# Performance work log

Hardware: AMD Instinct MI355X
Metric: run time of the kernel (lower is better)

Reference implementation:

```python
import jax, jax.numpy as jnp
import numpy as np

B, SQ, SKV, D = 4, 4096, 4096, 64

def setup_inputs() -> dict:
    key = jax.random.key(0)
    kq, kv = jax.random.split(key)
    query = jax.random.normal(kq, (B, SQ, D), dtype=jnp.float32)
    value = jax.random.normal(kv, (B, SKV, D), dtype=jnp.float32)
    return {"query": query, "value": value}

def reference(query, value):
    # scores = Q @ V^T  (value acts as both keys and values; no 1/sqrt(d) scaling)
    scores = jnp.einsum('bqd,bkd->bqk', query, value)  # [B, SQ, SKV]
    dist = jax.nn.softmax(scores, axis=-1)
    context = jnp.einsum('bqk,bkd->bqd', dist, value)  # [B, SQ, D]
    return context
```

## Files before the change

kernel.cpp:

```cpp
#include <hip/hip_runtime.h>
#include <type_traits>


#define NB   4
#define SQ   4096
#define SKV  4096
#define DH   64
#define L2E  1.44269504088896340736f

typedef _Float16 half8 __attribute__((ext_vector_type(8)));
typedef _Float16 half4 __attribute__((ext_vector_type(4)));
typedef _Float16 half2v __attribute__((ext_vector_type(2)));
typedef float f32x4 __attribute__((ext_vector_type(4)));
typedef unsigned short u16;

#define MFMA16(a, b, c) __builtin_amdgcn_mfma_f32_16x16x16f16((a), (b), (c), 0, 0, 0)
#define MFMA32(a, b, c) __builtin_amdgcn_mfma_f32_16x16x32_f16((a), (b), (c), 0, 0, 0)

__device__ __forceinline__ u16 f2h(float f) {
  _Float16 h = (_Float16)f;
  return __builtin_bit_cast(u16, h);
}
__device__ __forceinline__ half2v pkrtz(float a, float b) {
  return __builtin_bit_cast(half2v, __builtin_amdgcn_cvt_pkrtz(a, b));
}
__device__ __forceinline__ float fmax3(float a, float b, float c) {
  return fmaxf(fmaxf(a, b), c);
}

typedef __attribute__((address_space(1))) void gvoid;
typedef __attribute__((address_space(3))) void lvoid;
__device__ __forceinline__ void dma16(const u16* g, u16* l) {
  __builtin_amdgcn_global_load_lds((gvoid*)g, (lvoid*)l, 16, 0, 0);
}

__global__ __launch_bounds__(256) void prep_kernel(
    const float* __restrict__ V, u16* __restrict__ vh, u16* __restrict__ vt) {
  __shared__ u16 ldsT[16 * 72];
  int blk = blockIdx.x;
  int x   = blk & 7;
  int b   = x >> 1;
  int rem = ((x & 1) << 7) + (blk >> 3);
  int j0  = (rem >> 2) << 6;
  int d0  = (rem & 3) << 4;
  int t   = threadIdx.x;
  int j   = t >> 2;
  int dc  = (t & 3) << 2;

  const float* src = V + ((size_t)(b * SKV) + j0 + j) * DH + d0 + dc;
  float4 v4 = *(const float4*)src;
  u16 h[4] = {f2h(v4.x), f2h(v4.y), f2h(v4.z), f2h(v4.w)};
  unsigned p0 = (unsigned)h[0] | ((unsigned)h[1] << 16);
  unsigned p1 = (unsigned)h[2] | ((unsigned)h[3] << 16);
  int dfull = d0 + dc;
  int physd = ((((dfull >> 3) ^ (j & 7)) << 3)) + (dfull & 7);
  *(uint2*)(vh + ((size_t)(b * SKV) + j0 + j) * DH + physd) = make_uint2(p0, p1);

#pragma unroll
  for (int k = 0; k < 4; ++k) ldsT[(dc + k) * 72 + j] = h[k];
  __syncthreads();

  int dl = t >> 4;
  int jc = (t & 15) << 2;
  u16 tr[4];
#pragma unroll
  for (int k = 0; k < 4; ++k) tr[k] = ldsT[dl * 72 + jc + k];
  unsigned q0 = (unsigned)tr[0] | ((unsigned)tr[1] << 16);
  unsigned q1 = (unsigned)tr[2] | ((unsigned)tr[3] << 16);
  int d   = d0 + dl;
  int kc2 = jc >> 5;
  int g   = (jc >> 4) & 1;
  int qd  = (jc >> 2) & 3;
  int hp  = ((kc2 << 2) | qd) ^ (d & 7);
  *(uint2*)(vt + ((size_t)(b * DH) + d) * SKV + j0 + (hp << 3) + (g << 2)) =
      make_uint2(q0, q1);
}

__global__ __launch_bounds__(256, 4) void attn_kernel(
    const float* __restrict__ Q,
    const u16* __restrict__ vh,
    const u16* __restrict__ vt,
    u16* __restrict__ po,
    float* __restrict__ pm,
    float* __restrict__ pl,
    int S, int kvLen) {
  __shared__ __align__(16) u16 lds[2][2][4096];

  int blk  = blockIdx.x;
  int tile, s;
  if (S == 4) {
    int x  = blk & 7;
    int jj = ((x & 1) << 7) + (blk >> 3);
    tile   = ((x >> 1) << 6) + (jj >> 2);
    s      = jj & 3;
  } else {
    tile = blk / S;
    s    = blk - tile * S;
  }
  int b    = tile >> 6;
  int q0   = (tile & 63) << 6;
  int kv0  = s * kvLen;
  int t    = threadIdx.x;
  int wave = t >> 6;
  int lane = t & 63;
  int col  = lane & 15;
  int quad = lane >> 4;
  int qw   = q0 + (wave << 4);
  int c7   = col & 7;

  const u16* gv  = vh + (size_t)(b * SKV) * DH;
  const u16* gvt = vt + (size_t)(b * DH) * SKV;

  int r0 = t >> 3;
  int c0 = (t & 7) << 3;
  int wb = wave << 9;

  half8 qf[2];
#pragma unroll
  for (int kc = 0; kc < 2; ++kc) {
    const float* qp = Q + ((size_t)(b * SQ) + qw + col) * DH + kc * 32 + (quad << 3);
    float4 a0 = *(const float4*)qp;
    float4 a1 = *(const float4*)(qp + 4);
    half8 hq;
    hq[0] = (_Float16)(a0.x * L2E); hq[1] = (_Float16)(a0.y * L2E);
    hq[2] = (_Float16)(a0.z * L2E); hq[3] = (_Float16)(a0.w * L2E);
    hq[4] = (_Float16)(a1.x * L2E); hq[5] = (_Float16)(a1.y * L2E);
    hq[6] = (_Float16)(a1.z * L2E); hq[7] = (_Float16)(a1.w * L2E);
    qf[kc] = hq;
  }

  f32x4 o[4];
#pragma unroll
  for (int nf = 0; nf < 4; ++nf) o[nf] = (f32x4){0.f, 0.f, 0.f, 0.f};
  float m_r = -1e30f, l_r = 0.f;

  half4 pf[4];
  half8 vr[8];

  int ch0 = quad ^ c7;
  int ch1 = ch0 ^ 4;
  const char* Lb = (const char*)&lds[0][0][0];
  const char* a0p = Lb + (col << 7) + (ch0 << 4);
  const char* a1p = Lb + (col << 7) + (ch1 << 4);

  const u16* pvh  = gv + ((size_t)(kv0 + r0) << 6) + c0;
  const u16* pvh2 = pvh + 2048;
  const u16* pvt  = gvt + (size_t)r0 * SKV + kv0 + c0;
  const u16* pvt2 = pvt + (size_t)32 * SKV;

  dma16(pvh,  &lds[0][0][0] + wb);
  dma16(pvh2, &lds[0][0][0] + 2048 + wb);
  dma16(pvt,  &lds[0][1][0] + wb);
  dma16(pvt2, &lds[0][1][0] + 2048 + wb);
  pvh += 4096; pvh2 += 4096; pvt += 64; pvt2 += 64;

  int nIter = kvLen >> 6;

  auto body = [&](auto BUFC, int it_) {
    constexpr int BUF = decltype(BUFC)::value;
    constexpr int BO  = BUF * 16384;
    __syncthreads();

    if (it_ + 1 < nIter) {
      dma16(pvh,  &lds[BUF ^ 1][0][0] + wb);
      dma16(pvh2, &lds[BUF ^ 1][0][0] + 2048 + wb);
      dma16(pvt,  &lds[BUF ^ 1][1][0] + wb);
      dma16(pvt2, &lds[BUF ^ 1][1][0] + 2048 + wb);
    }
    pvh += 4096; pvh2 += 4096; pvt += 64; pvt2 += 64;

    f32x4 sf[4];
#pragma unroll
    for (int nf = 0; nf < 4; ++nf) sf[nf] = (f32x4){0.f, 0.f, 0.f, 0.f};
    __builtin_amdgcn_s_setprio(1);
#pragma unroll
    for (int nf = 0; nf < 4; ++nf) {
      half8 av0 = *(const half8*)(a0p + BO + nf * 2048);
      sf[nf] = MFMA32(av0, qf[0], sf[nf]);
      half8 av1 = *(const half8*)(a1p + BO + nf * 2048);
      sf[nf] = MFMA32(av1, qf[1], sf[nf]);
    }
    __builtin_amdgcn_s_setprio(0);

    float t0 = fmax3(sf[0][0], sf[0][1], sf[0][2]);
    float t1 = fmax3(sf[0][3], sf[1][0], sf[1][1]);
    float t2 = fmax3(sf[1][2], sf[1][3], sf[2][0]);
    float t3 = fmax3(sf[2][1], sf[2][2], sf[2][3]);
    float t4 = fmax3(sf[3][0], sf[3][1], sf[3][2]);
    float t5 = fmax3(t0, t1, sf[3][3]);
    float tmw = fmax3(t2, t3, t4);
    tmw = fmaxf(tmw, t5);
    float tx = __shfl_xor(tmw, 16, 64);

    if (it_ > 0) {
      __builtin_amdgcn_s_setprio(1);
#pragma unroll
      for (int nf2 = 0; nf2 < 4; ++nf2) {
        half8 w8 = vr[nf2];
        half4 wlo = __builtin_shufflevector(w8, w8, 0, 1, 2, 3);
        half4 whi = __builtin_shufflevector(w8, w8, 4, 5, 6, 7);
        o[nf2] = MFMA16(wlo, pf[0], o[nf2]);
        o[nf2] = MFMA16(whi, pf[1], o[nf2]);
      }
      __builtin_amdgcn_s_setprio(0);
    }

    float tm2 = fmaxf(tmw, tx);
    float ty = __shfl_xor(tm2, 32, 64);

    if (it_ > 0) {
      __builtin_amdgcn_s_setprio(1);
#pragma unroll
      for (int nf2 = 0; nf2 < 4; ++nf2) {
        half8 w8 = vr[4 + nf2];
        half4 wlo = __builtin_shufflevector(w8, w8, 0, 1, 2, 3);
        half4 whi = __builtin_shufflevector(w8, w8, 4, 5, 6, 7);
        o[nf2] = MFMA16(wlo, pf[2], o[nf2]);
        o[nf2] = MFMA16(whi, pf[3], o[nf2]);
      }
      __builtin_amdgcn_s_setprio(0);
    }

    {
      float tm = fmaxf(tm2, ty);
      float mn = fmaxf(m_r, tm);
      float al = 1.0f;
      bool need = !__all(mn == m_r);
      if (need) {
        al = exp2f(m_r - mn);
        m_r = mn;
      }
      float rs = 0.f;
#pragma unroll
      for (int nf = 0; nf < 4; ++nf) {
        float p0 = exp2f(sf[nf][0] - mn);
        float p1 = exp2f(sf[nf][1] - mn);
        float p2 = exp2f(sf[nf][2] - mn);
        float p3 = exp2f(sf[nf][3] - mn);
        rs += (p0 + p1) + (p2 + p3);
        half2v lo = pkrtz(p0, p1);
        half2v hi = pkrtz(p2, p3);
        pf[nf] = __builtin_shufflevector(lo, hi, 0, 1, 2, 3);
      }
      if (need) {
#pragma unroll
        for (int nf = 0; nf < 4; ++nf)
#pragma unroll
          for (int r = 0; r < 4; ++r) o[nf][r] *= al;
      }
      l_r = l_r * al + rs;
    }

#pragma unroll
    for (int nf2 = 0; nf2 < 4; ++nf2) {
      vr[nf2]     = *(const half8*)(a0p + BO + 8192 + nf2 * 2048);
      vr[4 + nf2] = *(const half8*)(a1p + BO + 8192 + nf2 * 2048);
    }
  };

  for (int it = 0; it < nIter; it += 2) {
    body(std::integral_constant<int, 0>{}, it);
    body(std::integral_constant<int, 1>{}, it + 1);
  }

  __builtin_amdgcn_s_setprio(1);
#pragma unroll
  for (int kc2 = 0; kc2 < 2; ++kc2) {
#pragma unroll
    for (int nf2 = 0; nf2 < 4; ++nf2) {
      half8 w8 = vr[kc2 * 4 + nf2];
      half4 wlo = __builtin_shufflevector(w8, w8, 0, 1, 2, 3);
      half4 whi = __builtin_shufflevector(w8, w8, 4, 5, 6, 7);
      o[nf2] = MFMA16(wlo, pf[kc2 * 2], o[nf2]);
      o[nf2] = MFMA16(whi, pf[kc2 * 2 + 1], o[nf2]);
    }
  }
  __builtin_amdgcn_s_setprio(0);

  l_r += __shfl_xor(l_r, 16, 64);
  l_r += __shfl_xor(l_r, 32, 64);
  int pidx = tile * S + s;
  if (quad == 0) {
    pm[(size_t)pidx * 64 + (wave << 4) + col] = m_r;
    pl[(size_t)pidx * 64 + (wave << 4) + col] = l_r;
  }

  __syncthreads();
  u16* tp = &lds[0][0][0];
  {
    int qrow = (wave << 4) + col;
#pragma unroll
    for (int nf2 = 0; nf2 < 4; ++nf2) {
#pragma unroll
      for (int r2 = 0; r2 < 4; r2 += 2) {
        unsigned pk = (unsigned)f2h(o[nf2][r2]) |
                      ((unsigned)f2h(o[nf2][r2 + 1]) << 16);
        int d = nf2 * 16 + (quad << 2) + r2;
        *(unsigned*)(tp + qrow * 72 + d) = pk;
      }
    }
  }
  __syncthreads();
  {
    u16* pob = po + (size_t)pidx * 64 * 64;
    int q = t >> 2, hc = (t & 3) << 4;
    uint4 x0 = *(const uint4*)(tp + q * 72 + hc);
    uint4 x1 = *(const uint4*)(tp + q * 72 + hc + 8);
    *(uint4*)(pob + q * 64 + hc)     = x0;
    *(uint4*)(pob + q * 64 + hc + 8) = x1;
  }
}

__global__ __launch_bounds__(256) void combine_kernel(
    const u16* __restrict__ po,
    const float* __restrict__ pm,
    const float* __restrict__ pl,
    float* __restrict__ out, int S) {
  int t    = threadIdx.x;
  int rowg;
  if (S == 4) {
    int x  = blockIdx.x & 7;
    int j2 = ((x & 1) << 6) + (blockIdx.x >> 3);
    int tile = ((x >> 1) << 6) + (j2 >> 1);
    rowg = tile * 64 + ((j2 & 1) << 5) + (t >> 3);
  } else {
    rowg = blockIdx.x * 32 + (t >> 3);
  }
  int tile = rowg >> 6;
  int row  = rowg & 63;
  int dc   = (t & 7) << 3;

  float mv[8], lv[8];
  float M = -1e30f;
#pragma unroll
  for (int s = 0; s < 8; ++s) {
    if (s < S) {
      mv[s] = pm[(size_t)(tile * S + s) * 64 + row];
      lv[s] = pl[(size_t)(tile * S + s) * 64 + row];
      M = fmaxf(M, mv[s]);
    }
  }
  float L = 0.f, w[8];
#pragma unroll
  for (int s = 0; s < 8; ++s) {
    if (s < S) {
      w[s] = exp2f(mv[s] - M);
      L += lv[s] * w[s];
    }
  }
  float acc[8] = {0.f, 0.f, 0.f, 0.f, 0.f, 0.f, 0.f, 0.f};
#pragma unroll
  for (int s = 0; s < 8; ++s) {
    if (s < S) {
      const u16* p = po + (size_t)(tile * S + s) * 4096 + row * 64 + dc;
      uint4 raw = *(const uint4*)p;
      half8 x = __builtin_bit_cast(half8, raw);
#pragma unroll
      for (int k = 0; k < 8; ++k) acc[k] += w[s] * (float)x[k];
    }
  }
  float invL = 1.0f / L;
  float* op = out + (size_t)rowg * 64 + dc;
  f32x4 o0 = (f32x4){acc[0], acc[1], acc[2], acc[3]};
  f32x4 o1 = (f32x4){acc[4], acc[5], acc[6], acc[7]};
  *(f32x4*)op       = o0 * invL;
  *(f32x4*)(op + 4) = o1 * invL;
}

extern "C" void kernel_launch(void* const* d_in, const int* in_sizes, int n_in,
                              void* d_out, int out_size, void* d_ws, size_t ws_size,
                              hipStream_t stream) {
  const float* Q = (const float*)d_in[0];
  const float* V = (const float*)d_in[1];
  float* out = (float*)d_out;

  const size_t convBytes = (size_t)2 * NB * SKV * DH * 2;
  auto partBytes = [](int S) {
    return (size_t)NB * 64 * S * ((size_t)64 * 64 * 2 + 64 * 8);
  };
  int S = 4;
  while (S > 1 && ws_size < convBytes + partBytes(S)) S >>= 1;
  int kvLen = SKV / S;

  u16* vh = (u16*)d_ws;
  u16* vt = vh + (size_t)NB * SKV * DH;
  u16* po = vt + (size_t)NB * SKV * DH;
  float* pm = (float*)(po + (size_t)NB * 64 * S * 64 * 64);
  float* pl = pm + (size_t)NB * 64 * S * 64;

  prep_kernel<<<NB * 256, 256, 0, stream>>>(V, vh, vt);
  attn_kernel<<<NB * 64 * S, 256, 0, stream>>>(Q, vh, vt, po, pm, pl, S, kvLen);
  combine_kernel<<<NB * SQ / 32, 256, 0, stream>>>(po, pm, pl, out, S);
}
```

Measured before the change: 105.4 us.

## Load K/V fragments directly from global into registers instead of LDS staging

Drops the double-buffered LDS staging of K and V tiles (global_load_lds DMA plus a barrier every iteration). Each wave now loads its own K and V MFMA fragments straight from global memory into registers, with the next K tile prefetched during the softmax step. This removes block-wide syncs and LDS traffic, but the four waves of a block now each load the same K/V data redundantly through the caches. Occupancy is lowered from 4 to 3 blocks per launch bound to leave room for the extra registers.

Measured after the change: 124.3 us. 17.9% more time.

```diff
diff --git a/kernel.cpp b/kernel.cpp
--- a/kernel.cpp
+++ b/kernel.cpp
@@ -1,5 +1,4 @@
 #include <hip/hip_runtime.h>
-#include <type_traits>
 
 
 #define NB   4
@@ -26,12 +25,6 @@
 }
 __device__ __forceinline__ float fmax3(float a, float b, float c) {
   return fmaxf(fmaxf(a, b), c);
-}
-
-typedef __attribute__((address_space(1))) void gvoid;
-typedef __attribute__((address_space(3))) void lvoid;
-__device__ __forceinline__ void dma16(const u16* g, u16* l) {
-  __builtin_amdgcn_global_load_lds((gvoid*)g, (lvoid*)l, 16, 0, 0);
 }
 
 __global__ __launch_bounds__(256) void prep_kernel(
@@ -76,7 +69,7 @@
       make_uint2(q0, q1);
 }
 
-__global__ __launch_bounds__(256, 4) void attn_kernel(
+__global__ __launch_bounds__(256, 3) void attn_kernel(
     const float* __restrict__ Q,
     const u16* __restrict__ vh,
     const u16* __restrict__ vt,
@@ -84,7 +77,7 @@
     float* __restrict__ pm,
     float* __restrict__ pl,
     int S, int kvLen) {
-  __shared__ __align__(16) u16 lds[2][2][4096];
+  __shared__ __align__(16) u16 tpl[64 * 72];
 
   int blk  = blockIdx.x;
   int tile, s;
@@ -107,13 +100,11 @@
   int quad = lane >> 4;
   int qw   = q0 + (wave << 4);
   int c7   = col & 7;
+  int ch0  = quad ^ c7;
+  int ch1  = ch0 ^ 4;
 
   const u16* gv  = vh + (size_t)(b * SKV) * DH;
   const u16* gvt = vt + (size_t)(b * DH) * SKV;
-
-  int r0 = t >> 3;
-  int c0 = (t & 7) << 3;
-  int wb = wave << 9;
 
   half8 qf[2];
 #pragma unroll
@@ -136,49 +127,31 @@
 
   half4 pf[4];
   half8 vr[8];
-
-  int ch0 = quad ^ c7;
-  int ch1 = ch0 ^ 4;
-  const char* Lb = (const char*)&lds[0][0][0];
-  const char* a0p = Lb + (col << 7) + (ch0 << 4);
-  const char* a1p = Lb + (col << 7) + (ch1 << 4);
-
-  const u16* pvh  = gv + ((size_t)(kv0 + r0) << 6) + c0;
-  const u16* pvh2 = pvh + 2048;
-  const u16* pvt  = gvt + (size_t)r0 * SKV + kv0 + c0;
-  const u16* pvt2 = pvt + (size_t)32 * SKV;
-
-  dma16(pvh,  &lds[0][0][0] + wb);
-  dma16(pvh2, &lds[0][0][0] + 2048 + wb);
-  dma16(pvt,  &lds[0][1][0] + wb);
-  dma16(pvt2, &lds[0][1][0] + 2048 + wb);
-  pvh += 4096; pvh2 += 4096; pvt += 64; pvt2 += 64;
+  half8 kr[8];
+
+  const u16* paw0 = gv + ((size_t)(kv0 + col) << 6) + (ch0 << 3);
+  const u16* paw1 = gv + ((size_t)(kv0 + col) << 6) + (ch1 << 3);
+  const u16* pvw0 = gvt + (size_t)col * SKV + kv0 + (ch0 << 3);
+  const u16* pvw1 = gvt + (size_t)col * SKV + kv0 + (ch1 << 3);
+
+#pragma unroll
+  for (int nf = 0; nf < 4; ++nf) {
+    kr[nf]     = *(const half8*)(paw0 + (nf << 10));
+    kr[4 + nf] = *(const half8*)(paw1 + (nf << 10));
+  }
+  paw0 += 4096; paw1 += 4096;
 
   int nIter = kvLen >> 6;
 
-  auto body = [&](auto BUFC, int it_) {
-    constexpr int BUF = decltype(BUFC)::value;
-    constexpr int BO  = BUF * 16384;
-    __syncthreads();
-
-    if (it_ + 1 < nIter) {
-      dma16(pvh,  &lds[BUF ^ 1][0][0] + wb);
-      dma16(pvh2, &lds[BUF ^ 1][0][0] + 2048 + wb);
-      dma16(pvt,  &lds[BUF ^ 1][1][0] + wb);
-      dma16(pvt2, &lds[BUF ^ 1][1][0] + 2048 + wb);
-    }
-    pvh += 4096; pvh2 += 4096; pvt += 64; pvt2 += 64;
-
+  for (int it = 0; it < nIter; ++it) {
     f32x4 sf[4];
 #pragma unroll
     for (int nf = 0; nf < 4; ++nf) sf[nf] = (f32x4){0.f, 0.f, 0.f, 0.f};
     __builtin_amdgcn_s_setprio(1);
 #pragma unroll
     for (int nf = 0; nf < 4; ++nf) {
-      half8 av0 = *(const half8*)(a0p + BO + nf * 2048);
-      sf[nf] = MFMA32(av0, qf[0], sf[nf]);
-      half8 av1 = *(const half8*)(a1p + BO + nf * 2048);
-      sf[nf] = MFMA32(av1, qf[1], sf[nf]);
+      sf[nf] = MFMA32(kr[nf],     qf[0], sf[nf]);
+      sf[nf] = MFMA32(kr[4 + nf], qf[1], sf[nf]);
     }
     __builtin_amdgcn_s_setprio(0);
 
@@ -192,7 +165,7 @@
     tmw = fmaxf(tmw, t5);
     float tx = __shfl_xor(tmw, 16, 64);
 
-    if (it_ > 0) {
+    if (it > 0) {
       __builtin_amdgcn_s_setprio(1);
 #pragma unroll
       for (int nf2 = 0; nf2 < 4; ++nf2) {
@@ -208,7 +181,7 @@
     float tm2 = fmaxf(tmw, tx);
     float ty = __shfl_xor(tm2, 32, 64);
 
-    if (it_ > 0) {
+    if (it > 0) {
       __builtin_amdgcn_s_setprio(1);
 #pragma unroll
       for (int nf2 = 0; nf2 < 4; ++nf2) {
@@ -220,6 +193,21 @@
       }
       __builtin_amdgcn_s_setprio(0);
     }
+
+#pragma unroll
+    for (int nf2 = 0; nf2 < 4; ++nf2) {
+      vr[nf2]     = *(const half8*)(pvw0 + nf2 * (16 * SKV));
+      vr[4 + nf2] = *(const half8*)(pvw1 + nf2 * (16 * SKV));
+    }
+    pvw0 += 64; pvw1 += 64;
+    if (it + 1 < nIter) {
+#pragma unroll
+      for (int nf = 0; nf < 4; ++nf) {
+        kr[nf]     = *(const half8*)(paw0 + (nf << 10));
+        kr[4 + nf] = *(const half8*)(paw1 + (nf << 10));
+      }
+    }
+    paw0 += 4096; paw1 += 4096;
 
     {
       float tm = fmaxf(tm2, ty);
@@ -250,17 +238,6 @@
       }
       l_r = l_r * al + rs;
     }
-
-#pragma unroll
-    for (int nf2 = 0; nf2 < 4; ++nf2) {
-      vr[nf2]     = *(const half8*)(a0p + BO + 8192 + nf2 * 2048);
-      vr[4 + nf2] = *(const half8*)(a1p + BO + 8192 + nf2 * 2048);
-    }
-  };
-
-  for (int it = 0; it < nIter; it += 2) {
-    body(std::integral_constant<int, 0>{}, it);
-    body(std::integral_constant<int, 1>{}, it + 1);
   }
 
   __builtin_amdgcn_s_setprio(1);
@@ -285,8 +262,6 @@
     pl[(size_t)pidx * 64 + (wave << 4) + col] = l_r;
   }
 
-  __syncthreads();
-  u16* tp = &lds[0][0][0];
   {
     int qrow = (wave << 4) + col;
 #pragma unroll
@@ -296,7 +271,7 @@
         unsigned pk = (unsigned)f2h(o[nf2][r2]) |
                       ((unsigned)f2h(o[nf2][r2 + 1]) << 16);
         int d = nf2 * 16 + (quad << 2) + r2;
-        *(unsigned*)(tp + qrow * 72 + d) = pk;
+        *(unsigned*)(tpl + qrow * 72 + d) = pk;
       }
     }
   }
@@ -304,8 +279,8 @@
   {
     u16* pob = po + (size_t)pidx * 64 * 64;
     int q = t >> 2, hc = (t & 3) << 4;
-    uint4 x0 = *(const uint4*)(tp + q * 72 + hc);
-    uint4 x1 = *(const uint4*)(tp + q * 72 + hc + 8);
+    uint4 x0 = *(const uint4*)(tpl + q * 72 + hc);
+    uint4 x1 = *(const uint4*)(tpl + q * 72 + hc + 8);
     *(uint4*)(pob + q * 64 + hc)     = x0;
     *(uint4*)(pob + q * 64 + hc + 8) = x1;
   }
```
